# Kernel tuning notes

Measured on AMD Instinct MI355X. Metric: run time of the kernel, lower is better.

Reference implementation:

```python
import jax, jax.numpy as jnp
import numpy as np

BASIS = 30
HIDDEN = 15
MAX_ATOMS = 30
NUM_ATOMS = 110
NUM_GAUSS = 56
T = 3
B = 2048


def setup_inputs() -> dict:
    key = jax.random.key(0)
    ks = jax.random.split(key, 16)
    Z = jax.random.randint(ks[0], (B, MAX_ATOMS), 0, NUM_ATOMS + 1)
    D = jax.random.uniform(ks[1], (B, MAX_ATOMS, MAX_ATOMS, NUM_GAUSS), dtype=jnp.float32)
    sizes = jax.random.randint(ks[2], (B,), 1, MAX_ATOMS + 1)
    s = 0.1
    C_embed = jax.random.normal(ks[3], (NUM_ATOMS + 1, BASIS), dtype=jnp.float32) * s
    df_w = jax.random.normal(ks[4], (NUM_GAUSS, BASIS), dtype=jnp.float32) * s
    df_b = jax.random.normal(ks[5], (BASIS,), dtype=jnp.float32) * s
    cf_w = jax.random.normal(ks[6], (BASIS, BASIS), dtype=jnp.float32) * s
    cf_b = jax.random.normal(ks[7], (BASIS,), dtype=jnp.float32) * s
    fc_w = jax.random.normal(ks[8], (BASIS, BASIS), dtype=jnp.float32) * s  # no bias
    mlp_w1 = jax.random.normal(ks[9], (BASIS, HIDDEN), dtype=jnp.float32) * s
    mlp_b1 = jax.random.normal(ks[10], (HIDDEN,), dtype=jnp.float32) * s
    mlp_w2 = jax.random.normal(ks[11], (HIDDEN, 1), dtype=jnp.float32) * s
    mlp_b2 = jax.random.normal(ks[12], (1,), dtype=jnp.float32) * s
    return {"Z": Z, "D": D, "sizes": sizes, "C_embed": C_embed, "df_w": df_w,
            "df_b": df_b, "cf_w": cf_w, "cf_b": cf_b, "fc_w": fc_w,
            "mlp_w1": mlp_w1, "mlp_b1": mlp_b1, "mlp_w2": mlp_w2, "mlp_b2": mlp_b2}


def reference(Z, D, sizes, C_embed, df_w, df_b, cf_w, cf_b, fc_w,
              mlp_w1, mlp_b1, mlp_w2, mlp_b2):
    # masks from sizes (mask_1d / mask_2d over max_atoms)
    ar = jnp.arange(MAX_ATOMS)
    m1 = (ar[None, :] < sizes[:, None]).astype(D.dtype)            # [B, A]
    m2 = m1[:, :, None] * m1[:, None, :]                           # [B, A, A]

    C = C_embed[Z]                                                 # [B, A, basis]
    d_hat = jnp.einsum('bijg,gk->bijk', D, df_w) + df_b            # [B, A, A, basis]

    for _ in range(T):
        X = C @ cf_w + cf_b                                        # [B, A, basis]
        X = X[:, :, None, :] * d_hat                               # [B, A, A, basis]
        X = jnp.tanh(jnp.einsum('bijh,hk->bijk', X, fc_w))         # [B, A, A, basis]
        C = C + (m2[..., None] * X).sum(axis=1)                    # sum over first atom axis

    E = jnp.tanh(C @ mlp_w1 + mlp_b1) @ mlp_w2 + mlp_b2            # [B, A, 1]
    E = E[..., 0]                                                  # [B, A]
    return (m1 * E).sum(axis=-1)                                   # [B]
```

## Files before the change

kernel.cpp:

```cpp
#include <hip/hip_runtime.h>
#include <hip/hip_bf16.h>

typedef __attribute__((ext_vector_type(8))) short bh8;
typedef __attribute__((ext_vector_type(4))) float f4;

#define MFMA_BF16 __builtin_amdgcn_mfma_f32_16x16x32_bf16

__device__ __forceinline__ float fast_tanh(float x) {
  float cl = fminf(fmaxf(x, -15.f), 15.f);
  float e = __builtin_amdgcn_exp2f(cl * 2.885390081777927f);
  return (e - 1.f) * __builtin_amdgcn_rcpf(e + 1.f);
}

__device__ __forceinline__ short bf16hi(float f, float* hf) {
  __hip_bfloat16 h = __float2bfloat16(f);
  *hf = __bfloat162float(h);
  short s;
  __builtin_memcpy(&s, &h, 2);
  return s;
}
__device__ __forceinline__ short bf16s(float f) {
  __hip_bfloat16 h = __float2bfloat16(f);
  short s;
  __builtin_memcpy(&s, &h, 2);
  return s;
}

__device__ __forceinline__ unsigned pack2_bf16(float a, float b) {
  unsigned ua = __float_as_uint(a);
  unsigned ub = __float_as_uint(b);
  ua = (ua + 0x7fffu + ((ua >> 16) & 1u)) >> 16;
  ub = (ub + 0x7fffu + ((ub >> 16) & 1u)) & 0xffff0000u;
  return ua | ub;
}


__global__ __launch_bounds__(256, 4) void mdtnn_phA_mfma(
    const float* __restrict__ Dg, const int* __restrict__ sizesg,
    const float* __restrict__ dfwg, const float* __restrict__ dfbg,
    uint2* __restrict__ dhg)
{
  const int b = blockIdx.x, tid = threadIdx.x;
  const int w = tid >> 6, l = tid & 63;
  const int lr = l & 15, lc = l >> 4;
  const int n = sizesg[b];
  const int nn = n * n;
  const unsigned inv = (65536u + (unsigned)n - 1) / (unsigned)n;

  bh8 Ah[2][2], Al[2][2];
  #pragma unroll
  for (int ht = 0; ht < 2; ++ht) {
    const int h = ht * 16 + lr;
    #pragma unroll
    for (int kc = 0; kc < 2; ++kc) {
      #pragma unroll
      for (int e = 0; e < 8; ++e) {
        const int g = kc * 32 + lc * 8 + e;
        float v = (g < 56 && h < 30) ? dfwg[g * 30 + h] : 0.f;
        float hf;
        Ah[ht][kc][e] = bf16hi(v, &hf);
        Al[ht][kc][e] = bf16s(v - hf);
      }
    }
  }
  float dfbv[2][4];
  #pragma unroll
  for (int ht = 0; ht < 2; ++ht)
    #pragma unroll
    for (int e = 0; e < 4; ++e) {
      const int h = ht * 16 + lc * 4 + e;
      dfbv[ht][e] = (h < 30) ? dfbg[h] : 0.f;
    }

  const float* Db = Dg + (size_t)b * (30 * 30 * 56);
  uint2* dhb = dhg + (size_t)b * (30 * 30 * 8);
  const f4 z4 = {0.f, 0.f, 0.f, 0.f};

  const int tiles = (nn + 15) >> 4;
  for (int t = w; t < tiles; t += 4) {
    const int p_raw = t * 16 + lr;
    const int p = min(p_raw, nn - 1);
    const int i = (int)(((unsigned)p * inv) >> 16);
    const int j = p - i * n;
    const int row = i * 30 + j;
    const float* Dp = Db + (size_t)row * 56;

    float4 q0 = *reinterpret_cast<const float4*>(Dp + lc * 8);
    float4 q1 = *reinterpret_cast<const float4*>(Dp + lc * 8 + 4);
    float4 q2 = {0.f, 0.f, 0.f, 0.f}, q3 = {0.f, 0.f, 0.f, 0.f};
    if (lc < 3) {
      q2 = *reinterpret_cast<const float4*>(Dp + 32 + lc * 8);
      q3 = *reinterpret_cast<const float4*>(Dp + 32 + lc * 8 + 4);
    }
    bh8 B0, B1;
    B0[0] = bf16s(q0.x); B0[1] = bf16s(q0.y); B0[2] = bf16s(q0.z); B0[3] = bf16s(q0.w);
    B0[4] = bf16s(q1.x); B0[5] = bf16s(q1.y); B0[6] = bf16s(q1.z); B0[7] = bf16s(q1.w);
    B1[0] = bf16s(q2.x); B1[1] = bf16s(q2.y); B1[2] = bf16s(q2.z); B1[3] = bf16s(q2.w);
    B1[4] = bf16s(q3.x); B1[5] = bf16s(q3.y); B1[6] = bf16s(q3.z); B1[7] = bf16s(q3.w);

    f4 a0 = z4, a1 = z4;
    a0 = MFMA_BF16(Al[0][0], B0, a0, 0, 0, 0);
    a0 = MFMA_BF16(Ah[0][0], B0, a0, 0, 0, 0);
    a0 = MFMA_BF16(Al[0][1], B1, a0, 0, 0, 0);
    a0 = MFMA_BF16(Ah[0][1], B1, a0, 0, 0, 0);
    a1 = MFMA_BF16(Al[1][0], B0, a1, 0, 0, 0);
    a1 = MFMA_BF16(Ah[1][0], B0, a1, 0, 0, 0);
    a1 = MFMA_BF16(Al[1][1], B1, a1, 0, 0, 0);
    a1 = MFMA_BF16(Ah[1][1], B1, a1, 0, 0, 0);

    if (p_raw < nn) {
      uint2 s0, s1;
      s0.x = pack2_bf16(a0[0] + dfbv[0][0], a0[1] + dfbv[0][1]);
      s0.y = pack2_bf16(a0[2] + dfbv[0][2], a0[3] + dfbv[0][3]);
      s1.x = pack2_bf16(a1[0] + dfbv[1][0], a1[1] + dfbv[1][1]);
      s1.y = pack2_bf16(a1[2] + dfbv[1][2], a1[3] + dfbv[1][3]);
      dhb[row * 8 + 0 * 4 + lc] = s0;
      dhb[row * 8 + 1 * 4 + lc] = s1;
    }
  }
}

__global__ __launch_bounds__(256, 4) void mdtnn_phB3(
    const int* __restrict__ Zg, const int* __restrict__ sizesg,
    const float* __restrict__ embg, const float* __restrict__ cfwg,
    const float* __restrict__ cfbg, const float* __restrict__ fcwg,
    const float* __restrict__ w1g, const float* __restrict__ b1g,
    const float* __restrict__ w2g, const float* __restrict__ b2g,
    const unsigned* __restrict__ dhg, float* __restrict__ outg, int Bn)
{
  const int tid = threadIdx.x;
  const int wid = tid >> 6, l = tid & 63;
  const int lr = l & 15, lc = l >> 4;
  const int bm = blockIdx.x * 4 + wid;

  __shared__ __align__(16) float buf[4][32][36];
  __shared__ __align__(16) float w1_s[32][16];
  __shared__ float b1_s[16], w2_s[16];

  for (int t = tid; t < 512; t += 256) {
    int k = t >> 4, c = t & 15;
    w1_s[k][c] = (k < 30 && c < 15) ? w1g[k * 15 + c] : 0.f;
  }
  if (tid < 16) {
    b1_s[tid] = (tid < 15) ? b1g[tid] : 0.f;
    w2_s[tid] = (tid < 15) ? w2g[tid] : 0.f;
  }
  __syncthreads();
  if (bm >= Bn) return;

  const int n = sizesg[bm];
  float (*mybuf)[36] = buf[wid];

  float fcwF0[8], fcwF1[8];
  bh8 cfwB0h, cfwB0l, cfwB1h, cfwB1l;
  #pragma unroll
  for (int e = 0; e < 8; ++e) {
    const int kk = lc * 8 + e;
    const int c1 = lr + 16;
    fcwF0[e] = (kk < 30) ? fcwg[kk * 30 + lr] : 0.f;
    fcwF1[e] = (kk < 30 && c1 < 30) ? fcwg[kk * 30 + c1] : 0.f;
    float g0 = (kk < 30) ? cfwg[kk * 30 + lr] : 0.f;
    float g1 = (kk < 30 && c1 < 30) ? cfwg[kk * 30 + c1] : 0.f;
    float hf;
    cfwB0h[e] = bf16hi(g0, &hf);
    cfwB0l[e] = bf16s(g0 - hf);
    cfwB1h[e] = bf16hi(g1, &hf);
    cfwB1l[e] = bf16s(g1 - hf);
  }
  const float cfb0 = cfbg[lr];
  const float cfb1 = (lr + 16 < 30) ? cfbg[lr + 16] : 0.f;

  f4 C00, C01, C10, C11;
  #pragma unroll
  for (int e = 0; e < 4; ++e) {
    const int r0 = lc * 4 + e;
    const int r1 = 16 + lc * 4 + e;
    const int z0 = Zg[bm * 30 + r0];
    C00[e] = embg[z0 * 30 + lr];
    C01[e] = (lr + 16 < 30) ? embg[z0 * 30 + lr + 16] : 0.f;
    if (r1 < 30) {
      const int z1 = Zg[bm * 30 + r1];
      C10[e] = embg[z1 * 30 + lr];
      C11[e] = (lr + 16 < 30) ? embg[z1 * 30 + lr + 16] : 0.f;
    } else {
      C10[e] = 0.f;
      C11[e] = 0.f;
    }
  }

  const unsigned* dhb = dhg + (size_t)bm * 14400;
  const f4 z4 = {0.f, 0.f, 0.f, 0.f};

  for (int it = 0; it < 3; ++it) {
    uint4 a0c = {0, 0, 0, 0}, a1c = {0, 0, 0, 0};
    if (lr < n)      a0c = *reinterpret_cast<const uint4*>(dhb + lr * 16 + lc * 4);
    if (lr + 16 < n) a1c = *reinterpret_cast<const uint4*>(dhb + lr * 16 + 256 + lc * 4);

    #pragma unroll
    for (int e = 0; e < 4; ++e) {
      mybuf[lc * 4 + e][lr]           = C00[e];
      mybuf[lc * 4 + e][lr + 16]      = C01[e];
      mybuf[16 + lc * 4 + e][lr]      = C10[e];
      mybuf[16 + lc * 4 + e][lr + 16] = C11[e];
    }
    float cv0[8], cv1[8];
    *reinterpret_cast<float4*>(&cv0[0]) = *reinterpret_cast<const float4*>(&mybuf[lr][lc * 8]);
    *reinterpret_cast<float4*>(&cv0[4]) = *reinterpret_cast<const float4*>(&mybuf[lr][lc * 8 + 4]);
    *reinterpret_cast<float4*>(&cv1[0]) = *reinterpret_cast<const float4*>(&mybuf[16 + lr][lc * 8]);
    *reinterpret_cast<float4*>(&cv1[4]) = *reinterpret_cast<const float4*>(&mybuf[16 + lr][lc * 8 + 4]);
    bh8 Ch0, Cl0, Ch1, Cl1;
    #pragma unroll
    for (int e = 0; e < 8; ++e) {
      float hf;
      Ch0[e] = bf16hi(cv0[e], &hf);
      Cl0[e] = bf16s(cv0[e] - hf);
      Ch1[e] = bf16hi(cv1[e], &hf);
      Cl1[e] = bf16s(cv1[e] - hf);
    }
    f4 d00 = MFMA_BF16(Ch0, cfwB0l, z4, 0, 0, 0);
    d00 = MFMA_BF16(Cl0, cfwB0h, d00, 0, 0, 0);
    d00 = MFMA_BF16(Ch0, cfwB0h, d00, 0, 0, 0);
    f4 d01 = MFMA_BF16(Ch0, cfwB1l, z4, 0, 0, 0);
    d01 = MFMA_BF16(Cl0, cfwB1h, d01, 0, 0, 0);
    d01 = MFMA_BF16(Ch0, cfwB1h, d01, 0, 0, 0);
    f4 d10 = MFMA_BF16(Ch1, cfwB0l, z4, 0, 0, 0);
    d10 = MFMA_BF16(Cl1, cfwB0h, d10, 0, 0, 0);
    d10 = MFMA_BF16(Ch1, cfwB0h, d10, 0, 0, 0);
    f4 d11 = MFMA_BF16(Ch1, cfwB1l, z4, 0, 0, 0);
    d11 = MFMA_BF16(Cl1, cfwB1h, d11, 0, 0, 0);
    d11 = MFMA_BF16(Ch1, cfwB1h, d11, 0, 0, 0);
    #pragma unroll
    for (int e = 0; e < 4; ++e) {
      mybuf[lc * 4 + e][lr]           = d00[e] + cfb0;
      mybuf[lc * 4 + e][lr + 16]      = d01[e] + cfb1;
      mybuf[16 + lc * 4 + e][lr]      = d10[e] + cfb0;
      mybuf[16 + lc * 4 + e][lr + 16] = d11[e] + cfb1;
    }

    f4 i00 = z4, i01 = z4, i10 = z4, i11 = z4;
    for (int i = 0; i < n; ++i) {
      uint4 a0n = {0, 0, 0, 0}, a1n = {0, 0, 0, 0};
      if (i + 1 < n) {
        const unsigned* p = dhb + (i + 1) * 480;
        if (lr < n)      a0n = *reinterpret_cast<const uint4*>(p + lr * 16 + lc * 4);
        if (lr + 16 < n) a1n = *reinterpret_cast<const uint4*>(p + lr * 16 + 256 + lc * 4);
      }
      float4 xA = *reinterpret_cast<const float4*>(&mybuf[i][lc * 8]);
      float4 xB = *reinterpret_cast<const float4*>(&mybuf[i][lc * 8 + 4]);
      float xv[8] = {xA.x, xA.y, xA.z, xA.w, xB.x, xB.y, xB.z, xB.w};
      bh8 W0, W1;
      #pragma unroll
      for (int e = 0; e < 8; ++e) {
        W0[e] = bf16s(xv[e] * fcwF0[e]);
        W1[e] = bf16s(xv[e] * fcwF1[e]);
      }
      const bh8 A0 = *reinterpret_cast<const bh8*>(&a0c);
      const bh8 A1 = *reinterpret_cast<const bh8*>(&a1c);
      f4 g;
      g = MFMA_BF16(A0, W0, z4, 0, 0, 0);
      #pragma unroll
      for (int e = 0; e < 4; ++e) i00[e] += fast_tanh(g[e]);
      g = MFMA_BF16(A0, W1, z4, 0, 0, 0);
      #pragma unroll
      for (int e = 0; e < 4; ++e) i01[e] += fast_tanh(g[e]);
      g = MFMA_BF16(A1, W0, z4, 0, 0, 0);
      #pragma unroll
      for (int e = 0; e < 4; ++e) i10[e] += fast_tanh(g[e]);
      g = MFMA_BF16(A1, W1, z4, 0, 0, 0);
      #pragma unroll
      for (int e = 0; e < 4; ++e) i11[e] += fast_tanh(g[e]);
      a0c = a0n;
      a1c = a1n;
    }
    C00 += i00;
    C01 += i01;
    C10 += i10;
    C11 += i11;
  }

  #pragma unroll
  for (int e = 0; e < 4; ++e) {
    mybuf[lc * 4 + e][lr]           = C00[e];
    mybuf[lc * 4 + e][lr + 16]      = C01[e];
    mybuf[16 + lc * 4 + e][lr]      = C10[e];
    mybuf[16 + lc * 4 + e][lr + 16] = C11[e];
  }
  float esum = 0.f;
  for (int t = l; t < n * 16; t += 64) {
    int j = t >> 4, c = t & 15;
    if (c < 15) {
      float a = b1_s[c];
      #pragma unroll
      for (int kc = 0; kc < 8; ++kc) {
        float4 c4 = *reinterpret_cast<const float4*>(&mybuf[j][kc * 4]);
        a = fmaf(c4.x, w1_s[kc * 4 + 0][c], a);
        a = fmaf(c4.y, w1_s[kc * 4 + 1][c], a);
        a = fmaf(c4.z, w1_s[kc * 4 + 2][c], a);
        a = fmaf(c4.w, w1_s[kc * 4 + 3][c], a);
      }
      esum += fast_tanh(a) * w2_s[c];
    }
  }
  #pragma unroll
  for (int off = 32; off; off >>= 1) esum += __shfl_down(esum, off);
  if (l == 0) outg[bm] = esum + (float)n * b2g[0];
}

extern "C" void kernel_launch(void* const* d_in, const int* in_sizes, int n_in,
                              void* d_out, int out_size, void* d_ws, size_t ws_size,
                              hipStream_t stream) {
  (void)in_sizes; (void)n_in; (void)ws_size;
  const int*   Z   = (const int*)d_in[0];
  const float* D   = (const float*)d_in[1];
  const int*   sz  = (const int*)d_in[2];
  const float* emb = (const float*)d_in[3];
  const float* dfw = (const float*)d_in[4];
  const float* dfb = (const float*)d_in[5];
  const float* cfw = (const float*)d_in[6];
  const float* cfb = (const float*)d_in[7];
  const float* fcw = (const float*)d_in[8];
  const float* w1  = (const float*)d_in[9];
  const float* b1  = (const float*)d_in[10];
  const float* w2  = (const float*)d_in[11];
  const float* b2  = (const float*)d_in[12];
  float* out = (float*)d_out;
  const int B = out_size;

  mdtnn_phA_mfma<<<dim3(B), dim3(256), 0, stream>>>(D, sz, dfw, dfb, (uint2*)d_ws);
  mdtnn_phB3<<<dim3((B + 3) / 4), dim3(256), 0, stream>>>(Z, sz, emb, cfw, cfb, fcw,
                                                          w1, b1, w2, b2,
                                                          (const unsigned*)d_ws, out, B);
}
```

Before: 123.2 us.

## Split per-molecule interaction loop across two waves with LDS reduction

Phase B now assigns one molecule to a 128-thread block of two wavefronts instead of four molecules per 256-thread block with one wave each. Each wave handles half of the i (first-atom) range of the sum, and the partial sums are combined through shared memory with barriers each iteration. The final energy MLP is also split across both waves. This gives twice as many waves per molecule, which shortens the serial critical path when there are few molecules per CU. The cost is extra barriers, a shared-memory reduction, and duplicated per-wave setup such as the cf_w GEMM.

```diff
diff --git a/kernel.cpp b/kernel.cpp
--- a/kernel.cpp
+++ b/kernel.cpp
@@ -120,24 +120,24 @@
   }
 }
 
-__global__ __launch_bounds__(256, 4) void mdtnn_phB3(
+__global__ __launch_bounds__(128, 3) void mdtnn_phB4(
     const int* __restrict__ Zg, const int* __restrict__ sizesg,
     const float* __restrict__ embg, const float* __restrict__ cfwg,
     const float* __restrict__ cfbg, const float* __restrict__ fcwg,
     const float* __restrict__ w1g, const float* __restrict__ b1g,
     const float* __restrict__ w2g, const float* __restrict__ b2g,
-    const unsigned* __restrict__ dhg, float* __restrict__ outg, int Bn)
+    const unsigned* __restrict__ dhg, float* __restrict__ outg)
 {
   const int tid = threadIdx.x;
   const int wid = tid >> 6, l = tid & 63;
   const int lr = l & 15, lc = l >> 4;
-  const int bm = blockIdx.x * 4 + wid;
-
-  __shared__ __align__(16) float buf[4][32][36];
+  const int bm = blockIdx.x;
+
+  __shared__ __align__(16) float buf[2][32][36];
   __shared__ __align__(16) float w1_s[32][16];
-  __shared__ float b1_s[16], w2_s[16];
-
-  for (int t = tid; t < 512; t += 256) {
+  __shared__ float b1_s[16], w2_s[16], wsum[2];
+
+  for (int t = tid; t < 512; t += 128) {
     int k = t >> 4, c = t & 15;
     w1_s[k][c] = (k < 30 && c < 15) ? w1g[k * 15 + c] : 0.f;
   }
@@ -145,8 +145,6 @@
     b1_s[tid] = (tid < 15) ? b1g[tid] : 0.f;
     w2_s[tid] = (tid < 15) ? w2g[tid] : 0.f;
   }
-  __syncthreads();
-  if (bm >= Bn) return;
 
   const int n = sizesg[bm];
   float (*mybuf)[36] = buf[wid];
@@ -189,12 +187,20 @@
   }
 
   const unsigned* dhb = dhg + (size_t)bm * 14400;
+  const int n0 = (n + 1) >> 1;
+  const int ibeg = wid ? n0 : 0;
+  const int iend = wid ? n : n0;
   const f4 z4 = {0.f, 0.f, 0.f, 0.f};
+
+  __syncthreads();
 
   for (int it = 0; it < 3; ++it) {
     uint4 a0c = {0, 0, 0, 0}, a1c = {0, 0, 0, 0};
-    if (lr < n)      a0c = *reinterpret_cast<const uint4*>(dhb + lr * 16 + lc * 4);
-    if (lr + 16 < n) a1c = *reinterpret_cast<const uint4*>(dhb + lr * 16 + 256 + lc * 4);
+    if (ibeg < iend) {
+      const unsigned* p = dhb + (size_t)ibeg * 480;
+      if (lr < n)      a0c = *reinterpret_cast<const uint4*>(p + lr * 16 + lc * 4);
+      if (lr + 16 < n) a1c = *reinterpret_cast<const uint4*>(p + lr * 16 + 256 + lc * 4);
+    }
 
     #pragma unroll
     for (int e = 0; e < 4; ++e) {
@@ -238,10 +244,10 @@
     }
 
     f4 i00 = z4, i01 = z4, i10 = z4, i11 = z4;
-    for (int i = 0; i < n; ++i) {
+    for (int i = ibeg; i < iend; ++i) {
       uint4 a0n = {0, 0, 0, 0}, a1n = {0, 0, 0, 0};
-      if (i + 1 < n) {
-        const unsigned* p = dhb + (i + 1) * 480;
+      if (i + 1 < iend) {
+        const unsigned* p = dhb + (size_t)(i + 1) * 480;
         if (lr < n)      a0n = *reinterpret_cast<const uint4*>(p + lr * 16 + lc * 4);
         if (lr + 16 < n) a1n = *reinterpret_cast<const uint4*>(p + lr * 16 + 256 + lc * 4);
       }
@@ -272,10 +278,27 @@
       a0c = a0n;
       a1c = a1n;
     }
-    C00 += i00;
-    C01 += i01;
-    C10 += i10;
-    C11 += i11;
+
+    #pragma unroll
+    for (int e = 0; e < 4; ++e) {
+      mybuf[lc * 4 + e][lr]           = i00[e];
+      mybuf[lc * 4 + e][lr + 16]      = i01[e];
+      mybuf[16 + lc * 4 + e][lr]      = i10[e];
+      mybuf[16 + lc * 4 + e][lr + 16] = i11[e];
+    }
+    __syncthreads();
+    #pragma unroll
+    for (int e = 0; e < 4; ++e) {
+      C00[e] += buf[0][lc * 4 + e][lr];
+      C00[e] += buf[1][lc * 4 + e][lr];
+      C01[e] += buf[0][lc * 4 + e][lr + 16];
+      C01[e] += buf[1][lc * 4 + e][lr + 16];
+      C10[e] += buf[0][16 + lc * 4 + e][lr];
+      C10[e] += buf[1][16 + lc * 4 + e][lr];
+      C11[e] += buf[0][16 + lc * 4 + e][lr + 16];
+      C11[e] += buf[1][16 + lc * 4 + e][lr + 16];
+    }
+    __syncthreads();
   }
 
   #pragma unroll
@@ -286,7 +309,7 @@
     mybuf[16 + lc * 4 + e][lr + 16] = C11[e];
   }
   float esum = 0.f;
-  for (int t = l; t < n * 16; t += 64) {
+  for (int t = l + wid * 64; t < n * 16; t += 128) {
     int j = t >> 4, c = t & 15;
     if (c < 15) {
       float a = b1_s[c];
@@ -303,7 +326,9 @@
   }
   #pragma unroll
   for (int off = 32; off; off >>= 1) esum += __shfl_down(esum, off);
-  if (l == 0) outg[bm] = esum + (float)n * b2g[0];
+  if (l == 0) wsum[wid] = esum;
+  __syncthreads();
+  if (tid == 0) outg[bm] = wsum[0] + wsum[1] + (float)n * b2g[0];
 }
 
 extern "C" void kernel_launch(void* const* d_in, const int* in_sizes, int n_in,
@@ -327,7 +352,7 @@
   const int B = out_size;
 
   mdtnn_phA_mfma<<<dim3(B), dim3(256), 0, stream>>>(D, sz, dfw, dfb, (uint2*)d_ws);
-  mdtnn_phB3<<<dim3((B + 3) / 4), dim3(256), 0, stream>>>(Z, sz, emb, cfw, cfb, fcw,
-                                                          w1, b1, w2, b2,
-                                                          (const unsigned*)d_ws, out, B);
-}
+  mdtnn_phB4<<<dim3(B), dim3(128), 0, stream>>>(Z, sz, emb, cfw, cfb, fcw,
+                                                w1, b1, w2, b2,
+                                                (const unsigned*)d_ws, out);
+}
```

After: 119.2 us. -3.3%, faster.
